# Performance work log

Measured on AMD Instinct MI355X. Metric: run time of the kernel, lower is better.

Reference implementation:

```python
import jax, jax.numpy as jnp
import numpy as np

HEADS = 16
DIM_HEAD = 64
SCALE = DIM_HEAD ** -0.5


def shift(x):
    # Transformer-XL relative shift trick. x: [..., i, j] -> [..., i, j]
    *pre, i, j = x.shape
    x = jnp.concatenate([x, jnp.zeros((*pre, i, i), x.dtype)], axis=-1)
    l = i + j - 1
    x = x.reshape(*pre, -1)
    pad = (-x.shape[-1]) % l
    x = jnp.concatenate([x, jnp.zeros((*pre, pad), x.dtype)], axis=-1)
    x = x.reshape(*pre, -1, l)
    return x[..., :i, i - 1:]


def setup_inputs() -> dict:
    key = jax.random.key(0)
    ks = jax.random.split(key, 8)
    b, t, e = 2, 1024, 1024
    mem_len, lmem_len = 1024, 128
    kv_len = t + mem_len + lmem_len
    return {
        "x": jax.random.normal(ks[0], (b, t, e), jnp.float32),
        "mem": jax.random.normal(ks[1], (b, mem_len, e), jnp.float32),
        "lmem": jax.random.normal(ks[2], (b, lmem_len, e), jnp.float32),
        "pos_emb": jax.random.normal(ks[3], (HEADS, kv_len, DIM_HEAD), jnp.float32),
        "input_mask": jnp.ones((b, t), bool),
        "Wq": jax.random.normal(ks[4], (e, e), jnp.float32) * 0.02,
        "Wkv": jax.random.normal(ks[5], (e, 2 * e), jnp.float32) * 0.02,
        "Wout": jax.random.normal(ks[6], (e, e), jnp.float32) * 0.02,
        "bout": jnp.zeros((e,), jnp.float32),
    }


def reference(x, mem, lmem, pos_emb, input_mask, Wq, Wkv, Wout, bout):
    b, t, e = x.shape
    h, dh = HEADS, DIM_HEAD
    mem_len, lmem_len = mem.shape[1], lmem.shape[1]
    total_mem = mem_len + lmem_len

    q = x @ Wq
    kv_input = jnp.concatenate([lmem, mem, x], axis=1)  # [b, kv_len, e]
    kv_len = kv_input.shape[1]
    k, v = jnp.split(kv_input @ Wkv, 2, axis=-1)

    def merge_heads(z):
        return z.reshape(b, -1, h, dh).transpose(0, 2, 1, 3)  # [b, h, n, dh]

    q, k, v = merge_heads(q), merge_heads(k), merge_heads(v)

    dots = jnp.einsum('bhid,bhjd->bhij', q, k) * SCALE  # [b, h, t, kv_len]

    pe = pos_emb[:, -kv_len:].astype(q.dtype)
    pos_dots = jnp.einsum('bhid,hjd->bhij', q, pe) * SCALE
    dots = dots + shift(pos_dots)

    mask_value = -jnp.finfo(dots.dtype).max

    pad_mask = input_mask[:, None, :, None] & input_mask[:, None, None, :]
    pad_mask = jnp.pad(pad_mask, ((0, 0), (0, 0), (0, 0), (total_mem, 0)), constant_values=True)
    dots = jnp.where(pad_mask, dots, mask_value)

    causal = jnp.triu(jnp.ones((t, t + total_mem), bool), k=1 + total_mem)
    dots = jnp.where(causal[None, None], mask_value, dots)

    attn = jax.nn.softmax(dots, axis=-1)
    out = jnp.einsum('bhij,bhjd->bhid', attn, v)
    out = out.transpose(0, 2, 1, 3).reshape(b, t, -1)
    return out @ Wout + bout
```

## Files before the change

### kernel.cpp

```cpp
#include <hip/hip_runtime.h>


typedef unsigned int   u32;
typedef unsigned short u16;
typedef unsigned long long u64;
typedef __attribute__((ext_vector_type(8))) short short8;
typedef __attribute__((ext_vector_type(4))) float f32x4;
typedef __attribute__((ext_vector_type(4))) u32   u32x4;

#define DEVI static __device__ __forceinline__
#define MFMA_BF16 __builtin_amdgcn_mfma_f32_16x16x32_bf16

DEVI u16 f2bf(float f) {
  u32 u = __builtin_bit_cast(u32, f);
  return (u16)((u + 0x7FFFu + ((u >> 16) & 1u)) >> 16);
}
DEVI float bf2f(u16 h) { u32 u = (u32)h << 16; return __builtin_bit_cast(float, u); }
DEVI u32 pk2(float lo, float hi) { return (u32)f2bf(lo) | ((u32)f2bf(hi) << 16); }
DEVI u32 cvtpk(float lo, float hi) {
  u32 r;
  asm("v_cvt_pk_bf16_f32 %0, %1, %2" : "=v"(r) : "v"(lo), "v"(hi));
  return r;
}
DEVI void gll16(const u16* g, u16* l) {
  __builtin_amdgcn_global_load_lds(
      (const __attribute__((address_space(1))) u32*)g,
      (__attribute__((address_space(3))) u32*)l, 16, 0, 0);
}

constexpr int T_ = 1024, E_ = 1024, KV = 2176, H_ = 16;
constexpr float QSCALE = 0.125f * 1.44269504088896f;

__global__ void k_prep_all(const float* __restrict__ x, const float* __restrict__ mem,
                           const float* __restrict__ lmem, const float* __restrict__ pos,
                           const float* __restrict__ Wq, const float* __restrict__ Wkv,
                           const float* __restrict__ Wout,
                           u16* __restrict__ kvin, u16* __restrict__ pe,
                           u16* __restrict__ WallT, u16* __restrict__ WoT) {
  __shared__ float tile[32][33];
  int bid = blockIdx.x, t = threadIdx.x;
  if (bid < 3264) {
    if (bid < 2176) {
      int u = bid * 256 + t;
      int b = u / (KV * E_ / 8);
      int r = u % (KV * E_ / 8);
      int j = r >> 7;
      int e8 = (r & 127) << 3;
      const float* src;
      if (j < 128)        src = lmem + ((size_t)(b * 128 + j) * E_ + e8);
      else if (j < 1152)  src = mem  + ((size_t)(b * 1024 + (j - 128)) * E_ + e8);
      else                src = x    + ((size_t)(b * 1024 + (j - 1152)) * E_ + e8);
      float4 a = ((const float4*)src)[0];
      float4 c = ((const float4*)src)[1];
      u32x4 o = { pk2(a.x, a.y), pk2(a.z, a.w), pk2(c.x, c.y), pk2(c.z, c.w) };
      *(u32x4*)(kvin + (size_t)u * 8) = o;
    } else {
      size_t u = (size_t)(bid - 2176) * 256 + t;
      float4 a = ((const float4*)(pos + u * 8))[0];
      float4 c = ((const float4*)(pos + u * 8))[1];
      u32x4 o = { pk2(a.x, a.y), pk2(a.z, a.w), pk2(c.x, c.y), pk2(c.z, c.w) };
      *(u32x4*)(pe + u * 8) = o;
    }
    return;
  }
  const float* src; u16* dst; int K, N, n0, k0;
  if (bid < 4288)      { int r = bid - 3264; src = Wq;   dst = WallT;             K = 1024; N = 1024; n0 = (r & 31) * 32; k0 = (r >> 5) * 32; }
  else if (bid < 6336) { int r = bid - 4288; src = Wkv;  dst = WallT + 1024*1024; K = 1024; N = 2048; n0 = (r & 63) * 32; k0 = (r >> 6) * 32; }
  else                 { int r = bid - 6336; src = Wout; dst = WoT;               K = 1024; N = 1024; n0 = (r & 31) * 32; k0 = (r >> 5) * 32; }
  int tx = t & 31, ty = t >> 5;
#pragma unroll
  for (int s = 0; s < 4; s++) tile[ty + 8 * s][tx] = src[(size_t)(k0 + ty + 8 * s) * N + n0 + tx];
  __syncthreads();
#pragma unroll
  for (int s = 0; s < 4; s++)
    dst[(size_t)(n0 + ty + 8 * s) * K + k0 + tx] = f2bf(tile[tx][ty + 8 * s]);
}

__global__ __launch_bounds__(256, 3)
void k_gemm_qkv(const u16* __restrict__ kvin, const u16* __restrict__ WallT,
                u16* __restrict__ qb, u16* __restrict__ kb, u16* __restrict__ vtb) {
  int bid = blockIdx.x;
  int b = bid / 336;
  int r = bid % 336;
  int nt, mt;
  if (r < 64) { nt = r >> 3; mt = 9 + (r & 7); }
  else { r -= 64; nt = 8 + r / 17; mt = r % 17; }

  const u16* A  = kvin + ((size_t)b * KV + (size_t)mt * 128) * E_;
  const u16* Bm = WallT + (size_t)nt * 128 * E_;

  __shared__ u16 As[2][128 * 32];
  __shared__ u16 Bs[2][128 * 32];

  int t = threadIdx.x;
  int wid = t >> 6, lane = t & 63;
  int wr = wid >> 1, wc = wid & 1;
  int l15 = lane & 15, l4 = lane >> 4;

  f32x4 acc[4][4] = {};

  int srowg = wid * 32 + (lane >> 2);
  int scol  = (lane & 3) * 8;
  auto stage = [&](int buf, int kt_) {
    int k0 = kt_ * 32;
    const u16* Ag = A  + (size_t)srowg * E_ + k0 + scol;
    const u16* Bg = Bm + (size_t)srowg * E_ + k0 + scol;
    u16* la = As[buf] + wid * 32 * 32;
    u16* lb = Bs[buf] + wid * 32 * 32;
    gll16(Ag, la);
    gll16(Ag + (size_t)16 * E_, la + 16 * 32);
    gll16(Bg, lb);
    gll16(Bg + (size_t)16 * E_, lb + 16 * 32);
  };

  stage(0, 0);
  for (int kt = 0; kt < 32; kt++) {
    __syncthreads();
    int buf = kt & 1;
    if (kt + 1 < 32) stage(buf ^ 1, kt + 1);
    short8 af[4], bfv[4];
#pragma unroll
    for (int m = 0; m < 4; m++)
      af[m] = *(const short8*)(As[buf] + (wr * 64 + m * 16 + l15) * 32 + l4 * 8);
#pragma unroll
    for (int n = 0; n < 4; n++)
      bfv[n] = *(const short8*)(Bs[buf] + (wc * 64 + n * 16 + l15) * 32 + l4 * 8);
#pragma unroll
    for (int m = 0; m < 4; m++)
#pragma unroll
      for (int n = 0; n < 4; n++)
        acc[m][n] = MFMA_BF16(af[m], bfv[n], acc[m][n], 0, 0, 0);
  }
  int grow_base = mt * 128 + wr * 64;
  int ncol_base = nt * 128 + wc * 64;
  if (nt < 8) {
#pragma unroll
    for (int m = 0; m < 4; m++)
#pragma unroll
      for (int n = 0; n < 4; n++) {
        int col = ncol_base + n * 16 + l15;
        int head = col >> 6, d = col & 63;
#pragma unroll
        for (int rg = 0; rg < 4; rg++) {
          int row = grow_base + m * 16 + l4 * 4 + rg - 1152;
          qb[(((size_t)b * 16 + head) * 1024 + row) * 64 + d] = f2bf(acc[m][n][rg] * QSCALE);
        }
      }
  } else if (nt < 16) {
#pragma unroll
    for (int m = 0; m < 4; m++)
#pragma unroll
      for (int n = 0; n < 4; n++) {
        int c = ncol_base + n * 16 + l15 - 1024;
        int head = c >> 6, d = c & 63;
#pragma unroll
        for (int rg = 0; rg < 4; rg++) {
          int row = grow_base + m * 16 + l4 * 4 + rg;
          kb[(((size_t)b * 16 + head) * KV + row) * 64 + d] = f2bf(acc[m][n][rg]);
        }
      }
  } else {
#pragma unroll
    for (int m = 0; m < 4; m++)
#pragma unroll
      for (int n = 0; n < 4; n++) {
        int c = ncol_base + n * 16 + l15 - 2048;
        int head = c >> 6, d = c & 63;
        int jb = grow_base + m * 16 + l4 * 4;
        u64 pv = (u64)f2bf(acc[m][n][0]) | ((u64)f2bf(acc[m][n][1]) << 16)
               | ((u64)f2bf(acc[m][n][2]) << 32) | ((u64)f2bf(acc[m][n][3]) << 48);
        *(u64*)(vtb + (((size_t)b * 16 + head) * 64 + d) * KV + jb) = pv;
      }
  }
}

__global__ __launch_bounds__(256, 2)
void k_attn(const u16* __restrict__ qb, const u16* __restrict__ kb,
            const u16* __restrict__ vtb, const u16* __restrict__ peb,
            u16* __restrict__ ao) {
  int bid = blockIdx.x;
  int xcd = bid & 7;
  int itr = (bid >> 3) & 15;
  int g   = bid >> 7;
  int it  = (g >= 2) ? (15 - itr) : itr;
  int bh = g * 8 + xcd;
  int b = bh >> 4, h = bh & 15;
  int i0 = it * 64;

  __shared__ u16 Klds[2][64][72];
  __shared__ u16 Vt[2][64][72];
  __shared__ u16 Band[64][136];
  __shared__ u16 Pb[4][16][72];

  int t = threadIdx.x, wid = t >> 6, lane = t & 63;
  int l15 = lane & 15, l4 = lane >> 4;
  int il = wid * 16 + l15;
  int srow = t >> 3, ssl = t & 7;

  const u16* kbase  = kb  + (size_t)bh * KV * 64;
  const u16* vtbase = vtb + (size_t)bh * 64 * KV;
  const u16* pebase = peb + (size_t)h * KV * 64;

  const u16* qptr = qb + ((size_t)bh * 1024 + i0 + il) * 64 + l4 * 8;
  short8 qf0 = *(const short8*)qptr;
  short8 qf1 = *(const short8*)(qptr + 32);

  f32x4 Of[4] = {};
  float mr = -1e30f, lr = 0.f;
  int njt = it + 19;

  u32x4 rk0, rk1, rv0, rv1;
  auto load_regs = [&](int jt_) {
    int j0_ = jt_ * 64;
    rk0 = *(const u32x4*)(kbase + (size_t)(j0_ + srow) * 64 + ssl * 8);
    rk1 = *(const u32x4*)(kbase + (size_t)(j0_ + srow + 32) * 64 + ssl * 8);
    rv0 = *(const u32x4*)(vtbase + (size_t)srow * KV + j0_ + ssl * 8);
    rv1 = *(const u32x4*)(vtbase + (size_t)(srow + 32) * KV + j0_ + ssl * 8);
  };
  auto store_tile = [&](int buf) {
    *(u32x4*)(&Klds[buf][srow][ssl * 8]) = rk0;
    *(u32x4*)(&Klds[buf][srow + 32][ssl * 8]) = rk1;
    *(u32x4*)(&Vt[buf][srow][ssl * 8]) = rv0;
    *(u32x4*)(&Vt[buf][srow + 32][ssl * 8]) = rv1;
  };
  auto load_pe = [&](int prb, short8* pf) {
#pragma unroll
    for (int rc = 0; rc < 4; rc++) {
      int rr = prb + rc * 16 + l15;
#pragma unroll
      for (int kk = 0; kk < 2; kk++)
        pf[rc * 2 + kk] = *(const short8*)(pebase + (size_t)rr * 64 + kk * 32 + l4 * 8);
    }
  };
  auto band_mfma_store = [&](int prb, const short8* pf) {
    f32x4 acc[4];
    __builtin_amdgcn_s_setprio(1);
#pragma unroll
    for (int rc = 0; rc < 4; rc++) {
      f32x4 a = {};
      a = MFMA_BF16(pf[rc * 2 + 0], qf0, a, 0, 0, 0);
      a = MFMA_BF16(pf[rc * 2 + 1], qf1, a, 0, 0, 0);
      acc[rc] = a;
    }
    __builtin_amdgcn_s_setprio(0);
#pragma unroll
    for (int rc = 0; rc < 4; rc++) {
      int rb = prb + rc * 16 + l4 * 4 + il + 1;
      u32 w01 = cvtpk(acc[rc][0], acc[rc][1]);
      u32 w23 = cvtpk(acc[rc][2], acc[rc][3]);
      Band[il][rb & 127]       = (u16)w01;
      Band[il][(rb + 1) & 127] = (u16)(w01 >> 16);
      Band[il][(rb + 2) & 127] = (u16)w23;
      Band[il][(rb + 3) & 127] = (u16)(w23 >> 16);
    }
  };
  auto band_ninf = [&](int prb) {
#pragma unroll
    for (int rc = 0; rc < 4; rc++) {
      int rb = prb + rc * 16 + l4 * 4 + il + 1;
#pragma unroll
      for (int rg = 0; rg < 4; rg++)
        Band[il][(rb + rg) & 127] = 0xFF80u;
    }
  };

  load_regs(0);
  store_tile(0);
  short8 pf[8];
  load_pe(960 - i0, pf);
  band_mfma_store(960 - i0, pf);
  load_pe(1024 - i0, pf);
  load_regs(1);

  int cur = 0;
  for (int jt = 0; jt < njt; jt++) {
    __syncthreads();

    f32x4 sc[4];
    __builtin_amdgcn_s_setprio(1);
#pragma unroll
    for (int jc = 0; jc < 4; jc++) {
      f32x4 a = {};
      short8 k0 = *(const short8*)(&Klds[cur][jc * 16 + l15][l4 * 8]);
      short8 k1 = *(const short8*)(&Klds[cur][jc * 16 + l15][32 + l4 * 8]);
      a = MFMA_BF16(k0, qf0, a, 0, 0, 0);
      a = MFMA_BF16(k1, qf1, a, 0, 0, 0);
      sc[jc] = a;
    }
    __builtin_amdgcn_s_setprio(0);

    if (jt == njt - 1) band_ninf(1024 + 64 * jt - i0);
    else               band_mfma_store(1024 + 64 * jt - i0, pf);
    if (jt + 2 < njt) load_pe(1024 + 64 * (jt + 1) - i0, pf);

    asm volatile("s_waitcnt lgkmcnt(0)" ::: "memory");
    __builtin_amdgcn_sched_barrier(0);

    float P[4][4];
    float mx = -1e30f;
    int cb0 = ((jt - it) & 1) << 6;
#pragma unroll
    for (int jc = 0; jc < 4; jc++) {
      u64 bl = *(const u64*)(&Band[il][cb0 + jc * 16 + l4 * 4]);
#pragma unroll
      for (int rg = 0; rg < 4; rg++) {
        float v = sc[jc][rg] + bf2f((u16)(bl >> (16 * rg)));
        P[jc][rg] = v;
        mx = fmaxf(mx, v);
      }
    }
    if (jt == 0) {
      mx = fmaxf(mx, __shfl_xor(mx, 16, 64));
      mx = fmaxf(mx, __shfl_xor(mx, 32, 64));
      mr = mx;
    }

    float ps = 0.f;
#pragma unroll
    for (int jc = 0; jc < 4; jc++) {
#pragma unroll
      for (int rg = 0; rg < 4; rg++) {
        float p = exp2f(P[jc][rg] - mr);
        P[jc][rg] = p;
        ps += p;
      }
      int cb = jc * 16 + l4 * 4;
      *(u32*)(&Pb[wid][l15][cb])     = cvtpk(P[jc][0], P[jc][1]);
      *(u32*)(&Pb[wid][l15][cb + 2]) = cvtpk(P[jc][2], P[jc][3]);
    }
    short8 vf[8];
#pragma unroll
    for (int df = 0; df < 4; df++)
#pragma unroll
      for (int kk = 0; kk < 2; kk++)
        vf[df * 2 + kk] = *(const short8*)(&Vt[cur][df * 16 + l15][kk * 32 + l4 * 8]);

    asm volatile("s_waitcnt lgkmcnt(0)" ::: "memory");
    __builtin_amdgcn_sched_barrier(0);

    short8 pB0 = *(const short8*)(&Pb[wid][l15][l4 * 8]);
    short8 pB1 = *(const short8*)(&Pb[wid][l15][32 + l4 * 8]);
    __builtin_amdgcn_s_setprio(1);
#pragma unroll
    for (int df = 0; df < 4; df++) {
      Of[df] = MFMA_BF16(vf[df * 2 + 0], pB0, Of[df], 0, 0, 0);
      Of[df] = MFMA_BF16(vf[df * 2 + 1], pB1, Of[df], 0, 0, 0);
    }
    __builtin_amdgcn_s_setprio(0);

    if (jt != 0) {
      mx = fmaxf(mx, __shfl_xor(mx, 16, 64));
      mx = fmaxf(mx, __shfl_xor(mx, 32, 64));
    }
    ps += __shfl_xor(ps, 16, 64);
    ps += __shfl_xor(ps, 32, 64);

    if (jt != 0 && !__all(mx <= mr + 8.0f)) {
      float mnew = fmaxf(mr, mx);
      float fac = exp2f(mr - mnew);
      mr = mnew;
      lr = (lr + ps) * fac;
#pragma unroll
      for (int df = 0; df < 4; df++) Of[df] *= fac;
    } else {
      lr += ps;
    }

    if (jt + 1 < njt) {
      store_tile(cur ^ 1);
      if (jt + 2 < njt) load_regs(jt + 2);
    }
    cur ^= 1;
  }

  float inv = 1.0f / lr;
  size_t ob = ((size_t)b * 1024 + i0 + il) * 1024 + h * 64;
#pragma unroll
  for (int df = 0; df < 4; df++) {
    u64 pv = (u64)f2bf(Of[df][0] * inv)         | ((u64)f2bf(Of[df][1] * inv) << 16)
           | ((u64)f2bf(Of[df][2] * inv) << 32) | ((u64)f2bf(Of[df][3] * inv) << 48);
    *(u64*)(ao + ob + df * 16 + l4 * 4) = pv;
  }
}

__global__ __launch_bounds__(256, 2)
void k_gemm_out(const u16* __restrict__ ao, const u16* __restrict__ WoT,
                const float* __restrict__ bias, float* __restrict__ out) {
  int mt = blockIdx.x & 31, nt = blockIdx.x >> 5;
  const u16* A  = ao  + (size_t)mt * 64 * E_;
  const u16* Bm = WoT + (size_t)nt * 128 * E_;
  __shared__ u16 As[2][64 * 40];
  __shared__ u16 Bs[2][128 * 40];
  int t = threadIdx.x, wid = t >> 6, lane = t & 63;
  int wr = wid >> 1, wc = wid & 1, l15 = lane & 15, l4 = lane >> 4;
  f32x4 acc[2][4] = {};
  int arow = t >> 2, aslot = t & 3;

  u32x4 ra, rb[2];
  auto ld = [&](int kt_) {
    int k0 = kt_ * 32;
    ra = *(const u32x4*)(A + (size_t)arow * E_ + k0 + aslot * 8);
#pragma unroll
    for (int p = 0; p < 2; p++)
      rb[p] = *(const u32x4*)(Bm + (size_t)(arow + 64 * p) * E_ + k0 + aslot * 8);
  };
  auto st = [&](int buf) {
    *(u32x4*)(As[buf] + arow * 40 + aslot * 8) = ra;
#pragma unroll
    for (int p = 0; p < 2; p++)
      *(u32x4*)(Bs[buf] + (arow + 64 * p) * 40 + aslot * 8) = rb[p];
  };

  ld(0); st(0); ld(1);
  for (int kt = 0; kt < 32; kt++) {
    __syncthreads();
    int buf = kt & 1;
    short8 af[2], bfv[4];
#pragma unroll
    for (int m = 0; m < 2; m++)
      af[m] = *(const short8*)(As[buf] + (wr * 32 + m * 16 + l15) * 40 + l4 * 8);
#pragma unroll
    for (int n = 0; n < 4; n++)
      bfv[n] = *(const short8*)(Bs[buf] + (wc * 64 + n * 16 + l15) * 40 + l4 * 8);
#pragma unroll
    for (int m = 0; m < 2; m++)
#pragma unroll
      for (int n = 0; n < 4; n++)
        acc[m][n] = MFMA_BF16(af[m], bfv[n], acc[m][n], 0, 0, 0);
    if (kt + 1 < 32) st(buf ^ 1);
    if (kt + 2 < 32) ld(kt + 2);
  }
#pragma unroll
  for (int n = 0; n < 4; n++) {
    int col = nt * 128 + wc * 64 + n * 16 + l15;
    float bv = bias[col];
#pragma unroll
    for (int m = 0; m < 2; m++) {
      int row = mt * 64 + wr * 32 + m * 16 + l4 * 4;
#pragma unroll
      for (int rg = 0; rg < 4; rg++)
        out[(size_t)(row + rg) * E_ + col] = acc[m][n][rg] + bv;
    }
  }
}

extern "C" void kernel_launch(void* const* d_in, const int* in_sizes, int n_in,
                              void* d_out, int out_size, void* d_ws, size_t ws_size,
                              hipStream_t stream) {
  (void)in_sizes; (void)n_in; (void)out_size; (void)ws_size;
  const float* x    = (const float*)d_in[0];
  const float* mem  = (const float*)d_in[1];
  const float* lmem = (const float*)d_in[2];
  const float* pos  = (const float*)d_in[3];
  const float* Wq   = (const float*)d_in[5];
  const float* Wkv  = (const float*)d_in[6];
  const float* Wout = (const float*)d_in[7];
  const float* bout = (const float*)d_in[8];
  float* out = (float*)d_out;

  u16* kvin  = (u16*)d_ws;
  u16* pe    = kvin  + (size_t)2 * KV * E_;
  u16* WallT = pe    + (size_t)H_ * KV * 64;
  u16* WoT   = WallT + (size_t)3072 * E_;
  u16* qb    = WoT   + (size_t)E_ * E_;
  u16* kb    = qb    + (size_t)2 * H_ * T_ * 64;
  u16* vtb   = kb    + (size_t)2 * H_ * KV * 64;
  u16* ao    = vtb   + (size_t)2 * H_ * KV * 64;

  k_prep_all<<<7360, 256, 0, stream>>>(x, mem, lmem, pos, Wq, Wkv, Wout,
                                       kvin, pe, WallT, WoT);
  k_gemm_qkv<<<672, 256, 0, stream>>>(kvin, WallT, qb, kb, vtb);
  k_attn<<<512, 256, 0, stream>>>(qb, kb, vtb, pe, ao);
  k_gemm_out<<<256, 256, 0, stream>>>(ao, WoT, bout, out);
}
```

Before: 128.7 us.

## Use direct global-to-LDS loads in output GEMM and tree-reduce softmax max/sum

The output projection GEMM now stages its A and B tiles with direct global-to-LDS loads (gll16) instead of going through registers, and drops the padded LDS row stride of 40 for an unpadded 32. This removes the register round-trip and the separate store step, at the cost of possible LDS bank conflicts on the MFMA fragment reads. The attention kernel's row max and row sum are also rewritten as tree reductions to shorten the serial dependency chains. The GEMM now loads one stage ahead after the barrier instead of two, which lowers prefetch depth. Relying on gll16 completion ordering with only a __syncthreads may be a correctness risk if no vmcnt wait is issued.

```diff
diff --git a/kernel.cpp b/kernel.cpp
--- a/kernel.cpp
+++ b/kernel.cpp
@@ -297,37 +297,35 @@
     __builtin_amdgcn_sched_barrier(0);
 
     float P[4][4];
-    float mx = -1e30f;
+    float mxj[4];
     int cb0 = ((jt - it) & 1) << 6;
 #pragma unroll
     for (int jc = 0; jc < 4; jc++) {
       u64 bl = *(const u64*)(&Band[il][cb0 + jc * 16 + l4 * 4]);
 #pragma unroll
-      for (int rg = 0; rg < 4; rg++) {
-        float v = sc[jc][rg] + bf2f((u16)(bl >> (16 * rg)));
-        P[jc][rg] = v;
-        mx = fmaxf(mx, v);
-      }
-    }
+      for (int rg = 0; rg < 4; rg++)
+        P[jc][rg] = sc[jc][rg] + bf2f((u16)(bl >> (16 * rg)));
+      mxj[jc] = fmaxf(fmaxf(P[jc][0], P[jc][1]), fmaxf(P[jc][2], P[jc][3]));
+    }
+    float mx = fmaxf(fmaxf(mxj[0], mxj[1]), fmaxf(mxj[2], mxj[3]));
     if (jt == 0) {
       mx = fmaxf(mx, __shfl_xor(mx, 16, 64));
       mx = fmaxf(mx, __shfl_xor(mx, 32, 64));
       mr = mx;
     }
 
-    float ps = 0.f;
+    float psj[4];
 #pragma unroll
     for (int jc = 0; jc < 4; jc++) {
 #pragma unroll
-      for (int rg = 0; rg < 4; rg++) {
-        float p = exp2f(P[jc][rg] - mr);
-        P[jc][rg] = p;
-        ps += p;
-      }
+      for (int rg = 0; rg < 4; rg++)
+        P[jc][rg] = exp2f(P[jc][rg] - mr);
+      psj[jc] = (P[jc][0] + P[jc][1]) + (P[jc][2] + P[jc][3]);
       int cb = jc * 16 + l4 * 4;
       *(u32*)(&Pb[wid][l15][cb])     = cvtpk(P[jc][0], P[jc][1]);
       *(u32*)(&Pb[wid][l15][cb + 2]) = cvtpk(P[jc][2], P[jc][3]);
     }
+    float ps = (psj[0] + psj[1]) + (psj[2] + psj[3]);
     short8 vf[8];
 #pragma unroll
     for (int df = 0; df < 4; df++)
@@ -389,46 +387,41 @@
   int mt = blockIdx.x & 31, nt = blockIdx.x >> 5;
   const u16* A  = ao  + (size_t)mt * 64 * E_;
   const u16* Bm = WoT + (size_t)nt * 128 * E_;
-  __shared__ u16 As[2][64 * 40];
-  __shared__ u16 Bs[2][128 * 40];
+  __shared__ u16 As[2][64 * 32];
+  __shared__ u16 Bs[2][128 * 32];
   int t = threadIdx.x, wid = t >> 6, lane = t & 63;
   int wr = wid >> 1, wc = wid & 1, l15 = lane & 15, l4 = lane >> 4;
   f32x4 acc[2][4] = {};
-  int arow = t >> 2, aslot = t & 3;
-
-  u32x4 ra, rb[2];
-  auto ld = [&](int kt_) {
+
+  int srA  = wid * 16 + (lane >> 2);
+  int srB  = wid * 32 + (lane >> 2);
+  int scol = (lane & 3) * 8;
+  auto stage = [&](int buf, int kt_) {
     int k0 = kt_ * 32;
-    ra = *(const u32x4*)(A + (size_t)arow * E_ + k0 + aslot * 8);
-#pragma unroll
-    for (int p = 0; p < 2; p++)
-      rb[p] = *(const u32x4*)(Bm + (size_t)(arow + 64 * p) * E_ + k0 + aslot * 8);
-  };
-  auto st = [&](int buf) {
-    *(u32x4*)(As[buf] + arow * 40 + aslot * 8) = ra;
-#pragma unroll
-    for (int p = 0; p < 2; p++)
-      *(u32x4*)(Bs[buf] + (arow + 64 * p) * 40 + aslot * 8) = rb[p];
-  };
-
-  ld(0); st(0); ld(1);
+    gll16(A  + (size_t)srA * E_ + k0 + scol, As[buf] + wid * 16 * 32);
+    const u16* Bg = Bm + (size_t)srB * E_ + k0 + scol;
+    u16* lb = Bs[buf] + wid * 32 * 32;
+    gll16(Bg, lb);
+    gll16(Bg + (size_t)16 * E_, lb + 16 * 32);
+  };
+
+  stage(0, 0);
   for (int kt = 0; kt < 32; kt++) {
     __syncthreads();
     int buf = kt & 1;
+    if (kt + 1 < 32) stage(buf ^ 1, kt + 1);
     short8 af[2], bfv[4];
 #pragma unroll
     for (int m = 0; m < 2; m++)
-      af[m] = *(const short8*)(As[buf] + (wr * 32 + m * 16 + l15) * 40 + l4 * 8);
+      af[m] = *(const short8*)(As[buf] + (wr * 32 + m * 16 + l15) * 32 + l4 * 8);
 #pragma unroll
     for (int n = 0; n < 4; n++)
-      bfv[n] = *(const short8*)(Bs[buf] + (wc * 64 + n * 16 + l15) * 40 + l4 * 8);
+      bfv[n] = *(const short8*)(Bs[buf] + (wc * 64 + n * 16 + l15) * 32 + l4 * 8);
 #pragma unroll
     for (int m = 0; m < 2; m++)
 #pragma unroll
       for (int n = 0; n < 4; n++)
         acc[m][n] = MFMA_BF16(af[m], bfv[n], acc[m][n], 0, 0, 0);
-    if (kt + 1 < 32) st(buf ^ 1);
-    if (kt + 2 < 32) ld(kt + 2);
   }
 #pragma unroll
   for (int n = 0; n < 4; n++) {
```

Result: slower. 134.9 us (+4.8%).
